# Optimization experiments

Hardware: AMD Instinct MI355X
Metric: run time of the kernel (lower is better)

## Reference

```python
import jax, jax.numpy as jnp
import numpy as np

N_NODES = 10000
N_EDGES = 160000
HIDDEN = 512
N_LAYERS = 5


def setup_inputs() -> dict:
    key = jax.random.key(0)
    ks = jax.random.split(key, 12)
    return {
        "feat": jax.random.normal(ks[0], (N_NODES, HIDDEN), dtype=jnp.float32),
        "adj_row": jax.random.randint(ks[1], (N_EDGES,), 0, N_NODES, dtype=jnp.int32),
        "adj_col": jax.random.randint(ks[2], (N_EDGES,), 0, N_NODES, dtype=jnp.int32),
        "adj_val": jax.random.uniform(ks[3], (N_EDGES,), dtype=jnp.float32),
        "Wg": jax.random.normal(ks[4], (N_LAYERS, HIDDEN, HIDDEN), dtype=jnp.float32) * 0.02,
        "bg": jnp.zeros((N_LAYERS, HIDDEN), dtype=jnp.float32),
        "vw1": jax.random.normal(ks[5], (HIDDEN, HIDDEN), dtype=jnp.float32) * 0.02,
        "vb1": jnp.zeros((HIDDEN,), dtype=jnp.float32),
        "vw2": jax.random.normal(ks[6], (HIDDEN, 1), dtype=jnp.float32) * 0.02,
        "vb2": jnp.zeros((1,), dtype=jnp.float32),
    }


def _spmm(adj_row, adj_col, adj_val, x, n):
    # out[r] = sum_e adj_val[e] * x[adj_col[e]] for edges with adj_row[e] == r
    gathered = adj_val[:, None] * x[adj_col]  # [E, H]
    return jax.ops.segment_sum(gathered, adj_row, num_segments=n)


def reference(feat, adj_row, adj_col, adj_val, Wg, bg, vw1, vb1, vw2, vb2):
    n = feat.shape[0]
    x = feat
    for i in range(N_LAYERS):  # 5 structurally identical GraphConv layers
        h = x @ Wg[i]                                 # dense GEMM [N,H]
        agg = _spmm(adj_row, adj_col, adj_val, h, n)  # sparse aggregation
        x = jax.nn.relu(agg + bg[i])                  # bias + ReLU (dropout = eval identity)
    h = jax.nn.relu(x @ vw1 + vb1)
    return jax.nn.sigmoid(h @ vw2 + vb2)  # [N, 1]
```

## Files before the change

kernel.cpp:

```cpp
#include <hip/hip_runtime.h>

#define H 512
#define NNODES 10000
#define NEDGES 160000
#define NLAYERS 5
#define TM 160
#define NMT 63

typedef __attribute__((ext_vector_type(8))) short short8;
typedef __attribute__((ext_vector_type(4))) float floatx4;

__device__ inline unsigned short f2bf(float v) {
    union { float f; unsigned int u; } x; x.f = v;
    unsigned int r = (x.u + 0x7fffu + ((x.u >> 16) & 1u)) >> 16;
    return (unsigned short)r;
}
__device__ inline float bf2f(unsigned short u) {
    union { unsigned int u; float f; } x; x.u = ((unsigned int)u) << 16; return x.f;
}
__device__ inline void gl_lds16(const void* g, void* l) {
    __builtin_amdgcn_global_load_lds((const __attribute__((address_space(1))) void*)g,
                                     (__attribute__((address_space(3))) void*)l, 16, 0, 0);
}

#define PB_ZERO1 79
#define PB_ZERO2 1875
#define PB_CVT   5000
#define PB_TR    1536
__global__ __launch_bounds__(256)
void fused_prep(int* __restrict__ counts, int* __restrict__ colsP,
                const float* __restrict__ feat, unsigned short* __restrict__ x,
                const float* __restrict__ Wg, const float* __restrict__ vw1,
                unsigned short* __restrict__ Wt) {
    const int b = blockIdx.x;
    const int t = threadIdx.x;
    if (b < PB_ZERO1) {
        int i = b * 256 + t;
        if (i < 20000) counts[i] = 0;
    } else if (b < PB_ZERO1 + PB_ZERO2) {
        int i = (b - PB_ZERO1) * 256 + t;
        if (i < 480000) colsP[i] = 0;
    } else if (b < PB_ZERO1 + PB_ZERO2 + PB_CVT) {
        int i = (b - PB_ZERO1 - PB_ZERO2) * 256 + t;
        if (i < NNODES * H / 4) {
            float4 v = ((const float4*)feat)[i];
            ushort4 o;
            o.x = f2bf(v.x); o.y = f2bf(v.y); o.z = f2bf(v.z); o.w = f2bf(v.w);
            ((ushort4*)x)[i] = o;
        }
    } else {
        __shared__ float tile[32][33];
        const int bb = b - PB_ZERO1 - PB_ZERO2 - PB_CVT;
        const int z = bb >> 8;
        const int rem = bb & 255;
        const int bx = (rem & 15) * 32;
        const int by = (rem >> 4) * 32;
        const float* in = (z < NLAYERS) ? (Wg + (size_t)z * H * H) : vw1;
        unsigned short* out = Wt + (size_t)z * H * H;
        const int tx = t & 31, ty = t >> 5;
        for (int i = ty; i < 32; i += 8)
            tile[i][tx] = in[(size_t)(by + i) * H + bx + tx];
        __syncthreads();
        for (int i = ty; i < 32; i += 8)
            out[(size_t)(bx + i) * H + by + tx] = f2bf(tile[tx][i]);
    }
}

__global__ void edge_hist(const int* __restrict__ rows, int* __restrict__ counts, int n) {
    int i = blockIdx.x * blockDim.x + threadIdx.x;
    if (i < n) atomicAdd(&counts[rows[i]], 1);
}

__global__ __launch_bounds__(1024)
void scan_rows_pad(const int* __restrict__ counts, int* __restrict__ row_ptr, int n) {
    __shared__ int sums[1024];
    const int t = threadIdx.x;
    const int base = t * 16;
    int local[16];
    int s = 0;
#pragma unroll
    for (int i = 0; i < 16; ++i) {
        int idx = base + i;
        int v = (idx < n) ? ((counts[idx] + 7) & ~7) : 0;
        local[i] = s;
        s += v;
    }
    sums[t] = s;
    __syncthreads();
    for (int off = 1; off < 1024; off <<= 1) {
        int v = (t >= off) ? sums[t - off] : 0;
        __syncthreads();
        sums[t] += v;
        __syncthreads();
    }
    const int prefix = (t == 0) ? 0 : sums[t - 1];
#pragma unroll
    for (int i = 0; i < 16; ++i) {
        int idx = base + i;
        if (idx < n) row_ptr[idx] = prefix + local[i];
    }
    if (t == 0) row_ptr[n] = sums[1023];
}

__global__ void edge_scatter(const int* __restrict__ rows, const int* __restrict__ colsin,
                             const float* __restrict__ valsin, const int* __restrict__ row_ptr,
                             int* __restrict__ fill, int* __restrict__ colsout,
                             float* __restrict__ valsout, int n) {
    int i = blockIdx.x * blockDim.x + threadIdx.x;
    if (i < n) {
        int r = rows[i];
        int pos = row_ptr[r] + atomicAdd(&fill[r], 1);
        colsout[pos] = colsin[i];
        valsout[pos] = valsin[i];
    }
}

__global__ __launch_bounds__(256)
void gemm_bf16_160(const unsigned short* __restrict__ A, const unsigned short* __restrict__ Bt,
                   unsigned short* __restrict__ C, const float* __restrict__ bias,
                   int has_bias_relu, int M) {
    __shared__ __align__(16) unsigned short lsA[TM * 64];
    __shared__ __align__(16) unsigned short lsB[64 * 64];
    const int L = blockIdx.x;
    const int ml = L & 7;
    const int rest = L >> 3;
    const int n = rest & 7;
    const int mh = rest >> 3;
    const int m = mh * 8 + ml;
    if (m >= NMT) return;
    const int tileM = m * TM;
    const int tileN = n * 64;

    const int t = threadIdx.x;
    const int lane = t & 63;
    const int wave = t >> 6;
    const int wm = wave >> 1, wn = wave & 1;
    const int quad = lane >> 4, r16 = lane & 15;

    floatx4 acc[5][2] = {};

    const unsigned short* ap[5];
#pragma unroll
    for (int q = 0; q < 5; ++q) {
        const int c = t + 256 * q;
        const int row = c >> 3;
        int g = tileM + row; if (g >= M) g = M - 1;
        ap[q] = A + (size_t)g * 512 + (((c & 7) ^ (row & 7)) * 8);
    }
    const unsigned short* bp[2];
#pragma unroll
    for (int q = 0; q < 2; ++q) {
        const int c = t + 256 * q;
        const int row = c >> 3;
        bp[q] = Bt + (size_t)(tileN + row) * 512 + (((c & 7) ^ (row & 7)) * 8);
    }

    for (int k0 = 0; k0 < 512; k0 += 64) {
#pragma unroll
        for (int q = 0; q < 5; ++q)
            gl_lds16(ap[q] + k0, lsA + (size_t)(t + 256 * q) * 8);
        gl_lds16(bp[0] + k0, lsB + (size_t)t * 8);
        gl_lds16(bp[1] + k0, lsB + (size_t)(t + 256) * 8);
        __syncthreads();

        short8 af[5][2], bfr[2][2];
#pragma unroll
        for (int i = 0; i < 5; ++i) {
            const int row = wm * 80 + i * 16 + r16;
#pragma unroll
            for (int kk = 0; kk < 2; ++kk) {
                const int kcw = kk * 4 + quad;
                af[i][kk] = *(const short8*)&lsA[(size_t)(row * 8 + (kcw ^ (row & 7))) * 8];
            }
        }
#pragma unroll
        for (int j = 0; j < 2; ++j) {
            const int row = wn * 32 + j * 16 + r16;
#pragma unroll
            for (int kk = 0; kk < 2; ++kk) {
                const int kcw = kk * 4 + quad;
                bfr[j][kk] = *(const short8*)&lsB[(size_t)(row * 8 + (kcw ^ (row & 7))) * 8];
            }
        }
#pragma unroll
        for (int kk = 0; kk < 2; ++kk)
#pragma unroll
            for (int i = 0; i < 5; ++i)
#pragma unroll
                for (int j = 0; j < 2; ++j)
                    acc[i][j] = __builtin_amdgcn_mfma_f32_16x16x32_bf16(af[i][kk], bfr[j][kk], acc[i][j], 0, 0, 0);
        __syncthreads();
    }

#pragma unroll
    for (int i = 0; i < 5; ++i) {
#pragma unroll
        for (int j = 0; j < 2; ++j) {
            const int col = tileN + wn * 32 + j * 16 + r16;
#pragma unroll
            for (int reg = 0; reg < 4; ++reg) {
                const int row = tileM + wm * 80 + i * 16 + quad * 4 + reg;
                if (row < M) {
                    float v = acc[i][j][reg];
                    if (has_bias_relu) { v += bias[col]; v = fmaxf(v, 0.f); }
                    C[(size_t)row * 512 + col] = f2bf(v);
                }
            }
        }
    }
}

__global__ __launch_bounds__(256)
void spmm_pad(const int* __restrict__ prow, const int* __restrict__ cols,
              const float* __restrict__ vals, const unsigned short* __restrict__ hmat,
              const float* __restrict__ bias, unsigned short* __restrict__ xout) {
    const int wave = threadIdx.x >> 6, lane = threadIdx.x & 63;
    const int r = blockIdx.x * 4 + wave;
    if (r >= NNODES) return;
    const int s = prow[r], e = prow[r + 1];
    const int cb = lane * 8;
    float acc[8] = {0.f, 0.f, 0.f, 0.f, 0.f, 0.f, 0.f, 0.f};

    for (int i = s; i < e; i += 8) {
        int c[8]; float v[8]; short8 g[8];
#pragma unroll
        for (int u = 0; u < 8; ++u) { c[u] = cols[i + u]; v[u] = vals[i + u]; }
#pragma unroll
        for (int u = 0; u < 8; ++u) g[u] = *(const short8*)(hmat + (size_t)c[u] * H + cb);
#pragma unroll
        for (int u = 0; u < 8; ++u)
#pragma unroll
            for (int j = 0; j < 8; ++j) acc[j] += v[u] * bf2f((unsigned short)g[u][j]);
    }

    short8 o;
#pragma unroll
    for (int j = 0; j < 8; ++j)
        o[j] = (short)f2bf(fmaxf(acc[j] + bias[cb + j], 0.f));
    *(short8*)(xout + (size_t)r * H + cb) = o;
}

__global__ __launch_bounds__(256)
void final_head(const unsigned short* __restrict__ h2, const float* __restrict__ w2,
                const float* __restrict__ b2, float* __restrict__ out, int n) {
    const int wave = threadIdx.x >> 6, lane = threadIdx.x & 63;
    const int r = blockIdx.x * 4 + wave;
    if (r >= n) return;
    const unsigned short* hrow = h2 + (size_t)r * H;
    float acc = 0.f;
#pragma unroll
    for (int i = 0; i < 8; ++i) {
        const int c = lane * 8 + i;
        acc += bf2f(hrow[c]) * w2[c];
    }
#pragma unroll
    for (int off = 32; off >= 1; off >>= 1) acc += __shfl_xor(acc, off, 64);
    if (lane == 0) out[r] = 1.f / (1.f + expf(-(acc + b2[0])));
}

extern "C" void kernel_launch(void* const* d_in, const int* in_sizes, int n_in,
                              void* d_out, int out_size, void* d_ws, size_t ws_size,
                              hipStream_t stream) {
    (void)in_sizes; (void)n_in; (void)out_size; (void)ws_size;
    const float* feat   = (const float*)d_in[0];
    const int* adj_row  = (const int*)d_in[1];
    const int* adj_col  = (const int*)d_in[2];
    const float* adj_val= (const float*)d_in[3];
    const float* Wg     = (const float*)d_in[4];
    const float* bg     = (const float*)d_in[5];
    const float* vw1    = (const float*)d_in[6];
    const float* vb1    = (const float*)d_in[7];
    const float* vw2    = (const float*)d_in[8];
    const float* vb2    = (const float*)d_in[9];
    float* out = (float*)d_out;

    char* ws = (char*)d_ws;
    unsigned short* x  = (unsigned short*)(ws + 0);
    unsigned short* h  = (unsigned short*)(ws + 10240000);
    unsigned short* Wt = (unsigned short*)(ws + 20480000);
    int*   prow    = (int*)(ws + 23625728);
    int*   counts  = (int*)(ws + 23785792);
    int*   fill    = (int*)(ws + 23825792);
    int*   colsP   = (int*)(ws + 23865792);
    float* valsP   = (float*)(ws + 24825792);

    fused_prep<<<PB_ZERO1 + PB_ZERO2 + PB_CVT + PB_TR, 256, 0, stream>>>(
        counts, colsP, feat, x, Wg, vw1, Wt);
    edge_hist<<<(NEDGES + 255) / 256, 256, 0, stream>>>(adj_row, counts, NEDGES);
    scan_rows_pad<<<1, 1024, 0, stream>>>(counts, prow, NNODES);
    edge_scatter<<<(NEDGES + 255) / 256, 256, 0, stream>>>(adj_row, adj_col, adj_val,
                                                           prow, fill, colsP, valsP, NEDGES);

    for (int l = 0; l < NLAYERS; ++l) {
        gemm_bf16_160<<<512, 256, 0, stream>>>(x, Wt + (size_t)l * H * H, h, nullptr, 0, NNODES);
        spmm_pad<<<(NNODES + 3) / 4, 256, 0, stream>>>(prow, colsP, valsP, h, bg + (size_t)l * H, x);
    }
    gemm_bf16_160<<<512, 256, 0, stream>>>(x, Wt + (size_t)NLAYERS * H * H, h, vb1, 1, NNODES);
    final_head<<<(NNODES + 3) / 4, 256, 0, stream>>>(h, vw2, vb2, out, NNODES);
}
```

Measured before the change: 328.0 us.

## Fuse edge histogram into first GEMM and split SpMM rows across two waves

The edge-count histogram now runs as extra blocks appended to the first layer's GEMM launch, which removes one kernel launch and lets the atomics overlap with GEMM work. The SpMM kernel now gives each row two waves, each covering half of the padded edge range, and combines the partial sums through shared memory. This doubles wave-level parallelism on the memory-bound gather at the cost of a block-wide barrier and an LDS reduction per row.

```diff
diff --git a/kernel.cpp b/kernel.cpp
--- a/kernel.cpp
+++ b/kernel.cpp
@@ -6,6 +6,7 @@
 #define NLAYERS 5
 #define TM 160
 #define NMT 63
+#define HISTB 625
 
 typedef __attribute__((ext_vector_type(8))) short short8;
 typedef __attribute__((ext_vector_type(4))) float floatx4;
@@ -66,11 +67,6 @@
     }
 }
 
-__global__ void edge_hist(const int* __restrict__ rows, int* __restrict__ counts, int n) {
-    int i = blockIdx.x * blockDim.x + threadIdx.x;
-    if (i < n) atomicAdd(&counts[rows[i]], 1);
-}
-
 __global__ __launch_bounds__(1024)
 void scan_rows_pad(const int* __restrict__ counts, int* __restrict__ row_ptr, int n) {
     __shared__ int sums[1024];
@@ -116,9 +112,15 @@
 }
 
 __global__ __launch_bounds__(256)
-void gemm_bf16_160(const unsigned short* __restrict__ A, const unsigned short* __restrict__ Bt,
-                   unsigned short* __restrict__ C, const float* __restrict__ bias,
-                   int has_bias_relu, int M) {
+void gemm_bf16_160h(const unsigned short* __restrict__ A, const unsigned short* __restrict__ Bt,
+                    unsigned short* __restrict__ C, const float* __restrict__ bias,
+                    int has_bias_relu, int M,
+                    const int* __restrict__ hrows, int* __restrict__ hcounts) {
+    if (blockIdx.x >= 512) {
+        const int i = (blockIdx.x - 512) * 256 + threadIdx.x;
+        if (i < NEDGES) atomicAdd(&hcounts[hrows[i]], 1);
+        return;
+    }
     __shared__ __align__(16) unsigned short lsA[TM * 64];
     __shared__ __align__(16) unsigned short lsB[64 * 64];
     const int L = blockIdx.x;
@@ -211,16 +213,23 @@
 }
 
 __global__ __launch_bounds__(256)
-void spmm_pad(const int* __restrict__ prow, const int* __restrict__ cols,
-              const float* __restrict__ vals, const unsigned short* __restrict__ hmat,
-              const float* __restrict__ bias, unsigned short* __restrict__ xout) {
+void spmm_split(const int* __restrict__ prow, const int* __restrict__ cols,
+                const float* __restrict__ vals, const unsigned short* __restrict__ hmat,
+                const float* __restrict__ bias, unsigned short* __restrict__ xout) {
+    __shared__ float red[2][64][8];
     const int wave = threadIdx.x >> 6, lane = threadIdx.x & 63;
-    const int r = blockIdx.x * 4 + wave;
-    if (r >= NNODES) return;
-    const int s = prow[r], e = prow[r + 1];
+    const int rowIdx = wave >> 1;
+    const int half = wave & 1;
+    const int r = blockIdx.x * 2 + rowIdx;
     const int cb = lane * 8;
+
+    const int s0 = prow[r], e0 = prow[r + 1];
+    const int nr = (e0 - s0) >> 3;
+    const int ra = (nr + 1) >> 1;
+    const int s = half ? (s0 + ra * 8) : s0;
+    const int e = half ? e0 : (s0 + ra * 8);
+
     float acc[8] = {0.f, 0.f, 0.f, 0.f, 0.f, 0.f, 0.f, 0.f};
-
     for (int i = s; i < e; i += 8) {
         int c[8]; float v[8]; short8 g[8];
 #pragma unroll
@@ -233,11 +242,20 @@
             for (int j = 0; j < 8; ++j) acc[j] += v[u] * bf2f((unsigned short)g[u][j]);
     }
 
-    short8 o;
-#pragma unroll
-    for (int j = 0; j < 8; ++j)
-        o[j] = (short)f2bf(fmaxf(acc[j] + bias[cb + j], 0.f));
-    *(short8*)(xout + (size_t)r * H + cb) = o;
+    if (half == 1) {
+#pragma unroll
+        for (int j = 0; j < 8; ++j) red[rowIdx][lane][j] = acc[j];
+    }
+    __syncthreads();
+    if (half == 0) {
+        short8 o;
+#pragma unroll
+        for (int j = 0; j < 8; ++j) {
+            float v = acc[j] + red[rowIdx][lane][j] + bias[cb + j];
+            o[j] = (short)f2bf(fmaxf(v, 0.f));
+        }
+        *(short8*)(xout + (size_t)r * H + cb) = o;
+    }
 }
 
 __global__ __launch_bounds__(256)
@@ -286,15 +304,21 @@
 
     fused_prep<<<PB_ZERO1 + PB_ZERO2 + PB_CVT + PB_TR, 256, 0, stream>>>(
         counts, colsP, feat, x, Wg, vw1, Wt);
-    edge_hist<<<(NEDGES + 255) / 256, 256, 0, stream>>>(adj_row, counts, NEDGES);
+
+    gemm_bf16_160h<<<512 + HISTB, 256, 0, stream>>>(x, Wt, h, nullptr, 0, NNODES,
+                                                    adj_row, counts);
     scan_rows_pad<<<1, 1024, 0, stream>>>(counts, prow, NNODES);
     edge_scatter<<<(NEDGES + 255) / 256, 256, 0, stream>>>(adj_row, adj_col, adj_val,
                                                            prow, fill, colsP, valsP, NEDGES);
-
-    for (int l = 0; l < NLAYERS; ++l) {
-        gemm_bf16_160<<<512, 256, 0, stream>>>(x, Wt + (size_t)l * H * H, h, nullptr, 0, NNODES);
-        spmm_pad<<<(NNODES + 3) / 4, 256, 0, stream>>>(prow, colsP, valsP, h, bg + (size_t)l * H, x);
-    }
-    gemm_bf16_160<<<512, 256, 0, stream>>>(x, Wt + (size_t)NLAYERS * H * H, h, vb1, 1, NNODES);
+    spmm_split<<<NNODES / 2, 256, 0, stream>>>(prow, colsP, valsP, h, bg, x);
+
+    for (int l = 1; l < NLAYERS; ++l) {
+        gemm_bf16_160h<<<512, 256, 0, stream>>>(x, Wt + (size_t)l * H * H, h, nullptr, 0,
+                                                NNODES, adj_row, counts);
+        spmm_split<<<NNODES / 2, 256, 0, stream>>>(prow, colsP, valsP, h,
+                                                   bg + (size_t)l * H, x);
+    }
+    gemm_bf16_160h<<<512, 256, 0, stream>>>(x, Wt + (size_t)NLAYERS * H * H, h, vb1, 1,
+                                            NNODES, adj_row, counts);
     final_head<<<(NNODES + 3) / 4, 256, 0, stream>>>(h, vw2, vb2, out, NNODES);
 }
```

Result: no change. 326.7 us (-0.4%).

## Pre-swizzle weights into MFMA fragments, interleave edge col/val, fold histogram into GEMM

Applied to the files above, without the earlier changes.

Weights are now converted once into an MFMA-fragment layout, so the GEMM loads B fragments straight from global memory into registers and no longer stages them through LDS. Edge columns and values are packed into int2 pairs so the SpMM needs one load per edge instead of two. The edge histogram is merged into the first GEMM launch as extra blocks, which removes one kernel launch. In exchange, B is read from global or L2 with no LDS reuse across waves, and the transpose in the prep kernel now uses strided scalar reads.

```diff
diff --git a/kernel.cpp b/kernel.cpp
--- a/kernel.cpp
+++ b/kernel.cpp
@@ -6,6 +6,7 @@
 #define NLAYERS 5
 #define TM 160
 #define NMT 63
+#define HISTB 625
 
 typedef __attribute__((ext_vector_type(8))) short short8;
 typedef __attribute__((ext_vector_type(4))) float floatx4;
@@ -26,12 +27,12 @@
 #define PB_ZERO1 79
 #define PB_ZERO2 1875
 #define PB_CVT   5000
-#define PB_TR    1536
+#define PB_WF    192
 __global__ __launch_bounds__(256)
-void fused_prep(int* __restrict__ counts, int* __restrict__ colsP,
+void fused_prep(int* __restrict__ counts, int* __restrict__ ev,
                 const float* __restrict__ feat, unsigned short* __restrict__ x,
                 const float* __restrict__ Wg, const float* __restrict__ vw1,
-                unsigned short* __restrict__ Wt) {
+                unsigned short* __restrict__ Wfrag) {
     const int b = blockIdx.x;
     const int t = threadIdx.x;
     if (b < PB_ZERO1) {
@@ -39,7 +40,7 @@
         if (i < 20000) counts[i] = 0;
     } else if (b < PB_ZERO1 + PB_ZERO2) {
         int i = (b - PB_ZERO1) * 256 + t;
-        if (i < 480000) colsP[i] = 0;
+        if (i < 480000) ev[i] = 0;
     } else if (b < PB_ZERO1 + PB_ZERO2 + PB_CVT) {
         int i = (b - PB_ZERO1 - PB_ZERO2) * 256 + t;
         if (i < NNODES * H / 4) {
@@ -49,26 +50,25 @@
             ((ushort4*)x)[i] = o;
         }
     } else {
-        __shared__ float tile[32][33];
         const int bb = b - PB_ZERO1 - PB_ZERO2 - PB_CVT;
-        const int z = bb >> 8;
-        const int rem = bb & 255;
-        const int bx = (rem & 15) * 32;
-        const int by = (rem >> 4) * 32;
+        const int z = bb >> 5;
+        const int rem = bb & 31;
         const float* in = (z < NLAYERS) ? (Wg + (size_t)z * H * H) : vw1;
-        unsigned short* out = Wt + (size_t)z * H * H;
-        const int tx = t & 31, ty = t >> 5;
-        for (int i = ty; i < 32; i += 8)
-            tile[i][tx] = in[(size_t)(by + i) * H + bx + tx];
-        __syncthreads();
-        for (int i = ty; i < 32; i += 8)
-            out[(size_t)(bx + i) * H + by + tx] = f2bf(tile[tx][i]);
-    }
-}
-
-__global__ void edge_hist(const int* __restrict__ rows, int* __restrict__ counts, int n) {
-    int i = blockIdx.x * blockDim.x + threadIdx.x;
-    if (i < n) atomicAdd(&counts[rows[i]], 1);
+        unsigned short* outp = Wfrag + ((size_t)(z * 32 + rem) * 8192);
+        const int colbase = rem * 16;
+#pragma unroll
+        for (int q = 0; q < 4; ++q) {
+            const int p = t + 256 * q;
+            const int ks = p >> 6, lane = p & 63;
+            const int col = colbase + (lane & 15);
+            const int kb = ks * 32 + (lane >> 4) * 8;
+            short8 o;
+#pragma unroll
+            for (int e = 0; e < 8; ++e)
+                o[e] = (short)f2bf(in[(size_t)(kb + e) * H + col]);
+            *(short8*)(outp + (size_t)p * 8) = o;
+        }
+    }
 }
 
 __global__ __launch_bounds__(1024)
@@ -104,23 +104,27 @@
 
 __global__ void edge_scatter(const int* __restrict__ rows, const int* __restrict__ colsin,
                              const float* __restrict__ valsin, const int* __restrict__ row_ptr,
-                             int* __restrict__ fill, int* __restrict__ colsout,
-                             float* __restrict__ valsout, int n) {
+                             int* __restrict__ fill, int2* __restrict__ ev, int n) {
     int i = blockIdx.x * blockDim.x + threadIdx.x;
     if (i < n) {
         int r = rows[i];
         int pos = row_ptr[r] + atomicAdd(&fill[r], 1);
-        colsout[pos] = colsin[i];
-        valsout[pos] = valsin[i];
+        int2 e; e.x = colsin[i]; e.y = __float_as_int(valsin[i]);
+        ev[pos] = e;
     }
 }
 
 __global__ __launch_bounds__(256)
-void gemm_bf16_160(const unsigned short* __restrict__ A, const unsigned short* __restrict__ Bt,
-                   unsigned short* __restrict__ C, const float* __restrict__ bias,
-                   int has_bias_relu, int M) {
+void gemm_bf16_160f(const unsigned short* __restrict__ A, const unsigned short* __restrict__ WfragZ,
+                    unsigned short* __restrict__ C, const float* __restrict__ bias,
+                    int has_bias_relu, int M,
+                    const int* __restrict__ hrows, int* __restrict__ hcounts) {
+    if (blockIdx.x >= 512) {
+        const int i = (blockIdx.x - 512) * 256 + threadIdx.x;
+        if (i < NEDGES) atomicAdd(&hcounts[hrows[i]], 1);
+        return;
+    }
     __shared__ __align__(16) unsigned short lsA[TM * 64];
-    __shared__ __align__(16) unsigned short lsB[64 * 64];
     const int L = blockIdx.x;
     const int ml = L & 7;
     const int rest = L >> 3;
@@ -147,23 +151,25 @@
         int g = tileM + row; if (g >= M) g = M - 1;
         ap[q] = A + (size_t)g * 512 + (((c & 7) ^ (row & 7)) * 8);
     }
-    const unsigned short* bp[2];
-#pragma unroll
-    for (int q = 0; q < 2; ++q) {
-        const int c = t + 256 * q;
-        const int row = c >> 3;
-        bp[q] = Bt + (size_t)(tileN + row) * 512 + (((c & 7) ^ (row & 7)) * 8);
-    }
-
-    for (int k0 = 0; k0 < 512; k0 += 64) {
+    const unsigned short* bbase[2];
+#pragma unroll
+    for (int j = 0; j < 2; ++j)
+        bbase[j] = WfragZ + ((size_t)(n * 4 + wn * 2 + j) * 16) * 512 + lane * 8;
+
+    for (int it = 0; it < 8; ++it) {
+        const int k0 = it * 64;
 #pragma unroll
         for (int q = 0; q < 5; ++q)
             gl_lds16(ap[q] + k0, lsA + (size_t)(t + 256 * q) * 8);
-        gl_lds16(bp[0] + k0, lsB + (size_t)t * 8);
-        gl_lds16(bp[1] + k0, lsB + (size_t)(t + 256) * 8);
+        short8 bfr[2][2];
+#pragma unroll
+        for (int j = 0; j < 2; ++j)
+#pragma unroll
+            for (int kk = 0; kk < 2; ++kk)
+                bfr[j][kk] = *(const short8*)(bbase[j] + (size_t)(it * 2 + kk) * 512);
         __syncthreads();
 
-        short8 af[5][2], bfr[2][2];
+        short8 af[5][2];
 #pragma unroll
         for (int i = 0; i < 5; ++i) {
             const int row = wm * 80 + i * 16 + r16;
@@ -171,15 +177,6 @@
             for (int kk = 0; kk < 2; ++kk) {
                 const int kcw = kk * 4 + quad;
                 af[i][kk] = *(const short8*)&lsA[(size_t)(row * 8 + (kcw ^ (row & 7))) * 8];
-            }
-        }
-#pragma unroll
-        for (int j = 0; j < 2; ++j) {
-            const int row = wn * 32 + j * 16 + r16;
-#pragma unroll
-            for (int kk = 0; kk < 2; ++kk) {
-                const int kcw = kk * 4 + quad;
-                bfr[j][kk] = *(const short8*)&lsB[(size_t)(row * 8 + (kcw ^ (row & 7))) * 8];
             }
         }
 #pragma unroll
@@ -211,8 +208,8 @@
 }
 
 __global__ __launch_bounds__(256)
-void spmm_pad(const int* __restrict__ prow, const int* __restrict__ cols,
-              const float* __restrict__ vals, const unsigned short* __restrict__ hmat,
+void spmm_pad(const int* __restrict__ prow, const int2* __restrict__ ev,
+              const unsigned short* __restrict__ hmat,
               const float* __restrict__ bias, unsigned short* __restrict__ xout) {
     const int wave = threadIdx.x >> 6, lane = threadIdx.x & 63;
     const int r = blockIdx.x * 4 + wave;
@@ -222,15 +219,17 @@
     float acc[8] = {0.f, 0.f, 0.f, 0.f, 0.f, 0.f, 0.f, 0.f};
 
     for (int i = s; i < e; i += 8) {
-        int c[8]; float v[8]; short8 g[8];
-#pragma unroll
-        for (int u = 0; u < 8; ++u) { c[u] = cols[i + u]; v[u] = vals[i + u]; }
-#pragma unroll
-        for (int u = 0; u < 8; ++u) g[u] = *(const short8*)(hmat + (size_t)c[u] * H + cb);
-#pragma unroll
-        for (int u = 0; u < 8; ++u)
-#pragma unroll
-            for (int j = 0; j < 8; ++j) acc[j] += v[u] * bf2f((unsigned short)g[u][j]);
+        int2 cv[8]; short8 g[8];
+#pragma unroll
+        for (int u = 0; u < 8; ++u) cv[u] = ev[i + u];
+#pragma unroll
+        for (int u = 0; u < 8; ++u) g[u] = *(const short8*)(hmat + (size_t)cv[u].x * H + cb);
+#pragma unroll
+        for (int u = 0; u < 8; ++u) {
+            const float v = __int_as_float(cv[u].y);
+#pragma unroll
+            for (int j = 0; j < 8; ++j) acc[j] += v * bf2f((unsigned short)g[u][j]);
+        }
     }
 
     short8 o;
@@ -275,26 +274,31 @@
     float* out = (float*)d_out;
 
     char* ws = (char*)d_ws;
-    unsigned short* x  = (unsigned short*)(ws + 0);
-    unsigned short* h  = (unsigned short*)(ws + 10240000);
-    unsigned short* Wt = (unsigned short*)(ws + 20480000);
+    unsigned short* x     = (unsigned short*)(ws + 0);
+    unsigned short* h     = (unsigned short*)(ws + 10240000);
+    unsigned short* Wfrag = (unsigned short*)(ws + 20480000);
     int*   prow    = (int*)(ws + 23625728);
     int*   counts  = (int*)(ws + 23785792);
     int*   fill    = (int*)(ws + 23825792);
-    int*   colsP   = (int*)(ws + 23865792);
-    float* valsP   = (float*)(ws + 24825792);
-
-    fused_prep<<<PB_ZERO1 + PB_ZERO2 + PB_CVT + PB_TR, 256, 0, stream>>>(
-        counts, colsP, feat, x, Wg, vw1, Wt);
-    edge_hist<<<(NEDGES + 255) / 256, 256, 0, stream>>>(adj_row, counts, NEDGES);
+    int*   ev      = (int*)(ws + 23865792);
+
+    fused_prep<<<PB_ZERO1 + PB_ZERO2 + PB_CVT + PB_WF, 256, 0, stream>>>(
+        counts, ev, feat, x, Wg, vw1, Wfrag);
+
+    gemm_bf16_160f<<<512 + HISTB, 256, 0, stream>>>(x, Wfrag, h, nullptr, 0, NNODES,
+                                                    adj_row, counts);
     scan_rows_pad<<<1, 1024, 0, stream>>>(counts, prow, NNODES);
     edge_scatter<<<(NEDGES + 255) / 256, 256, 0, stream>>>(adj_row, adj_col, adj_val,
-                                                           prow, fill, colsP, valsP, NEDGES);
-
-    for (int l = 0; l < NLAYERS; ++l) {
-        gemm_bf16_160<<<512, 256, 0, stream>>>(x, Wt + (size_t)l * H * H, h, nullptr, 0, NNODES);
-        spmm_pad<<<(NNODES + 3) / 4, 256, 0, stream>>>(prow, colsP, valsP, h, bg + (size_t)l * H, x);
-    }
-    gemm_bf16_160<<<512, 256, 0, stream>>>(x, Wt + (size_t)NLAYERS * H * H, h, vb1, 1, NNODES);
+                                                           prow, fill, (int2*)ev, NEDGES);
+    spmm_pad<<<(NNODES + 3) / 4, 256, 0, stream>>>(prow, (const int2*)ev, h, bg, x);
+
+    for (int l = 1; l < NLAYERS; ++l) {
+        gemm_bf16_160f<<<512, 256, 0, stream>>>(x, Wfrag + (size_t)l * H * H, h, nullptr, 0,
+                                                NNODES, adj_row, counts);
+        spmm_pad<<<(NNODES + 3) / 4, 256, 0, stream>>>(prow, (const int2*)ev, h,
+                                                       bg + (size_t)l * H, x);
+    }
+    gemm_bf16_160f<<<512, 256, 0, stream>>>(x, Wfrag + (size_t)NLAYERS * H * H, h, vb1, 1,
+                                            NNODES, adj_row, counts);
     final_head<<<(NNODES + 3) / 4, 256, 0, stream>>>(h, vw2, vb2, out, NNODES);
 }
```

New measurement: 332.9 us. Within noise of the previous version (+1.5%).
